# Performance work log

Measured on AMD Instinct MI355X. Metric: run time of the kernel, lower is better.

## Reference

```python
import jax, jax.numpy as jnp
import numpy as np

N, IN_CAPS, IN_LEN = 32, 1152, 32
OUT_CAPS, OUT_LEN = 64, 32
NUM_ITERATIONS = 3


def setup_inputs() -> dict:
    key = jax.random.key(0)
    k1, k2 = jax.random.split(key)
    x = jax.random.normal(k1, (N, IN_CAPS, IN_LEN), dtype=jnp.float32)
    # learnable weight, torch.randn init: (out_capsules, out_length, in_length)
    weight = jax.random.normal(k2, (OUT_CAPS, OUT_LEN, IN_LEN), dtype=jnp.float32)
    return {"x": x, "weight": weight}


def _squash(v):
    # v * ||v|| / (1 + ||v||^2)  ==  (||v||^2/(1+||v||^2)) * v/||v||
    norm_sq = jnp.sum(v * v, axis=-1, keepdims=True)
    norm = jnp.sqrt(norm_sq)
    return v * norm / (1.0 + norm_sq)


def reference(x, weight):
    # priors u_hat: [N, out_caps, in_caps, out_len]
    priors = jnp.einsum('oli,bni->bonl', weight, x)
    logits = jnp.zeros_like(priors)
    output = None
    for r in range(NUM_ITERATIONS):
        # coupling coefficients: softmax over output capsules (axis=1)
        probs = jax.nn.softmax(logits, axis=1)
        # weighted sum over input capsules -> [N, out_caps, 1, out_len]
        output = jnp.sum(probs * priors, axis=-2, keepdims=True)
        if r != NUM_ITERATIONS - 1:
            output = _squash(output)
            # agreement update: [N, out_caps, in_caps, 1]
            logits = logits + jnp.sum(priors * output, axis=-1, keepdims=True)
    output = _squash(output)  # squash=True default
    return jnp.squeeze(output, axis=-2)  # [N, out_caps, out_len]
```

## Files before the change

### kernel.cpp

```cpp
#include <hip/hip_runtime.h>
#include <math.h>


#define N_B      32
#define IN_CAPS  1152
#define IN_LEN   32
#define OUT_CAPS 64
#define OUT_LEN  32

#define NCHUNK 16
#define NPB    (IN_CAPS / NCHUNK)
#define PASS_WAVES 4
#define NPW    (NPB / PASS_WAVES)

#define DPPV(v, ctrl) \
    __int_as_float(__builtin_amdgcn_update_dpp(0, __float_as_int(v), ctrl, 0xF, 0xF, true))

__device__ __forceinline__ float wave_max(float v) {
    v = fmaxf(v, DPPV(v, 0xB1));
    v = fmaxf(v, DPPV(v, 0x4E));
    v = fmaxf(v, DPPV(v, 0x141));
    v = fmaxf(v, DPPV(v, 0x140));
    v = fmaxf(v, __shfl_xor(v, 16, 64));
    v = fmaxf(v, __shfl_xor(v, 32, 64));
    return v;
}
__device__ __forceinline__ float wave_sum(float v) {
    v += DPPV(v, 0xB1);
    v += DPPV(v, 0x4E);
    v += DPPV(v, 0x141);
    v += DPPV(v, 0x140);
    v += __shfl_xor(v, 16, 64);
    v += __shfl_xor(v, 32, 64);
    return v;
}

__global__ __launch_bounds__(256) void k_init(const float* __restrict__ x,
                                              const float* __restrict__ W,
                                              float* __restrict__ T) {
    const int b   = blockIdx.x;
    const int tid = threadIdx.x;
    const float* xb = x + (size_t)b * IN_CAPS * IN_LEN;

    __shared__ float4 red4[32][8];
    {
        const int q = tid & 7;
        const int g = tid >> 3;
        float4 acc = make_float4(0.f, 0.f, 0.f, 0.f);
        for (int n = g; n < IN_CAPS; n += 32) {
            const float4 v = *(const float4*)(xb + n * IN_LEN + q * 4);
            acc.x += v.x; acc.y += v.y; acc.z += v.z; acc.w += v.w;
        }
        red4[g][q] = acc;
    }
    __syncthreads();
    __shared__ float s0[IN_LEN];
    if (tid < 8) {
        float4 v = make_float4(0.f, 0.f, 0.f, 0.f);
        for (int g = 0; g < 32; ++g) {
            const float4 r = red4[g][tid];
            v.x += r.x; v.y += r.y; v.z += r.z; v.w += r.w;
        }
        const float inv = 1.f / 64.f;
        s0[tid * 4 + 0] = v.x * inv;
        s0[tid * 4 + 1] = v.y * inv;
        s0[tid * 4 + 2] = v.z * inv;
        s0[tid * 4 + 3] = v.w * inv;
    }
    __syncthreads();

    __shared__ float u[OUT_CAPS * OUT_LEN];
    for (int e = tid; e < OUT_CAPS * OUT_LEN; e += 256) {
        const float* wrow = W + (size_t)e * IN_LEN;
        float a = 0.f;
#pragma unroll
        for (int i = 0; i < IN_LEN; ++i) a = fmaf(wrow[i], s0[i], a);
        u[e] = a;
    }
    __syncthreads();

    __shared__ float scale[OUT_CAPS];
    if (tid < OUT_CAPS) {
        float ns = 0.f;
#pragma unroll
        for (int l = 0; l < OUT_LEN; ++l) { const float v = u[tid * OUT_LEN + l]; ns = fmaf(v, v, ns); }
        scale[tid] = sqrtf(ns) / (1.f + ns);
    }
    __syncthreads();

    for (int e = tid; e < OUT_CAPS * IN_LEN; e += 256) {
        const int o = e >> 5, i = e & 31;
        float a = 0.f;
#pragma unroll
        for (int l = 0; l < OUT_LEN; ++l)
            a = fmaf(W[((size_t)o * OUT_LEN + l) * IN_LEN + i], u[o * OUT_LEN + l], a);
        T[(size_t)b * OUT_CAPS * IN_LEN + e] = a * scale[o];
    }
}

__global__ __launch_bounds__(256, 2) void k_pass(const float* __restrict__ x,
                                                 const float* __restrict__ T,
                                                 float* __restrict__ part) {
    const int b    = blockIdx.x >> 4;
    const int c    = blockIdx.x & (NCHUNK - 1);
    const int tid  = threadIdx.x;
    const int lane = tid & 63;
    const int wave = __builtin_amdgcn_readfirstlane(tid >> 6);

    float t[IN_LEN];
    {
        const float4* Trow4 = (const float4*)(T + ((size_t)b * OUT_CAPS + lane) * IN_LEN);
#pragma unroll
        for (int q = 0; q < 8; ++q) {
            const float4 v = Trow4[q];
            t[4 * q] = v.x; t[4 * q + 1] = v.y; t[4 * q + 2] = v.z; t[4 * q + 3] = v.w;
        }
    }
    asm volatile("" : "+v"(t[0]), "+v"(t[1]), "+v"(t[2]), "+v"(t[3]),
                      "+v"(t[4]), "+v"(t[5]), "+v"(t[6]), "+v"(t[7]),
                      "+v"(t[8]), "+v"(t[9]), "+v"(t[10]), "+v"(t[11]),
                      "+v"(t[12]), "+v"(t[13]), "+v"(t[14]), "+v"(t[15]));
    asm volatile("" : "+v"(t[16]), "+v"(t[17]), "+v"(t[18]), "+v"(t[19]),
                      "+v"(t[20]), "+v"(t[21]), "+v"(t[22]), "+v"(t[23]),
                      "+v"(t[24]), "+v"(t[25]), "+v"(t[26]), "+v"(t[27]),
                      "+v"(t[28]), "+v"(t[29]), "+v"(t[30]), "+v"(t[31]));

    float s[IN_LEN];
#pragma unroll
    for (int i = 0; i < IN_LEN; ++i) s[i] = 0.f;

    const float* xw = x + ((size_t)b * IN_CAPS + c * NPB + wave * NPW) * IN_LEN;

#define L4(acc, R, k) \
    acc = fmaf((R).x, t[k],     acc); acc = fmaf((R).y, t[k + 1], acc); \
    acc = fmaf((R).z, t[k + 2], acc); acc = fmaf((R).w, t[k + 3], acc);
#define S4(R, k) \
    s[k]     = fmaf(prob, (R).x, s[k]);     s[k + 1] = fmaf(prob, (R).y, s[k + 1]); \
    s[k + 2] = fmaf(prob, (R).z, s[k + 2]); s[k + 3] = fmaf(prob, (R).w, s[k + 3]);

#pragma unroll
    for (int j = 0; j < NPW; ++j) {
        const float4* xr = (const float4*)(xw + j * IN_LEN);
        const float4 r0 = xr[0], r1 = xr[1], r2 = xr[2], r3 = xr[3],
                     r4 = xr[4], r5 = xr[5], r6 = xr[6], r7 = xr[7];

        float l0 = 0.f, l1 = 0.f, l2 = 0.f, l3 = 0.f;
        L4(l0, r0, 0)  L4(l1, r1, 4)  L4(l2, r2, 8)  L4(l3, r3, 12)
        L4(l0, r4, 16) L4(l1, r5, 20) L4(l2, r6, 24) L4(l3, r7, 28)
        const float logit = (l0 + l1) + (l2 + l3);

        const float m = wave_max(logit);
        const float p = __expf(logit - m);
        const float S = wave_sum(p);
        const float prob = p * __builtin_amdgcn_rcpf(S);

        S4(r0, 0)  S4(r1, 4)  S4(r2, 8)  S4(r3, 12)
        S4(r4, 16) S4(r5, 20) S4(r6, 24) S4(r7, 28)
    }
#undef L4
#undef S4

    __shared__ __align__(16) float sp[PASS_WAVES][OUT_CAPS][36];
    {
        float4* dst = (float4*)&sp[wave][lane][0];
#pragma unroll
        for (int q = 0; q < 8; ++q)
            dst[q] = make_float4(s[4 * q], s[4 * q + 1], s[4 * q + 2], s[4 * q + 3]);
    }
    __syncthreads();
    {
        float4* pb4 = (float4*)(part + ((size_t)b * NCHUNK + c) * OUT_CAPS * IN_LEN);
        for (int e = tid; e < OUT_CAPS * IN_LEN / 4; e += 256) {
            const int o = e >> 3, q4 = (e & 7) * 4;
            const float4 a0 = *(const float4*)&sp[0][o][q4];
            const float4 a1 = *(const float4*)&sp[1][o][q4];
            const float4 a2 = *(const float4*)&sp[2][o][q4];
            const float4 a3 = *(const float4*)&sp[3][o][q4];
            pb4[e] = make_float4(a0.x + a1.x + a2.x + a3.x,
                                 a0.y + a1.y + a2.y + a3.y,
                                 a0.z + a1.z + a2.z + a3.z,
                                 a0.w + a1.w + a2.w + a3.w);
        }
    }
}

__global__ __launch_bounds__(256) void k_vt(const float* __restrict__ W,
                                            const float* __restrict__ part,
                                            float* __restrict__ T,
                                            float* __restrict__ out,
                                            int final_iter) {
    const int b   = blockIdx.x;
    const int tid = threadIdx.x;

    __shared__ float s_lds[OUT_CAPS * IN_LEN];
    {
        const float4* pb4 = (const float4*)(part + (size_t)b * NCHUNK * OUT_CAPS * IN_LEN);
        for (int e = tid; e < OUT_CAPS * IN_LEN / 4; e += 256) {
            float4 acc = make_float4(0.f, 0.f, 0.f, 0.f);
#pragma unroll
            for (int c = 0; c < NCHUNK; ++c) {
                const float4 v = pb4[c * (OUT_CAPS * IN_LEN / 4) + e];
                acc.x += v.x; acc.y += v.y; acc.z += v.z; acc.w += v.w;
            }
            ((float4*)s_lds)[e] = acc;
        }
    }
    __syncthreads();

    __shared__ float u[OUT_CAPS * OUT_LEN];
    for (int e = tid; e < OUT_CAPS * OUT_LEN; e += 256) {
        const int o = e >> 5;
        const float* wrow = W + (size_t)e * IN_LEN;
        const float* srow = s_lds + o * IN_LEN;
        float a = 0.f;
#pragma unroll
        for (int i = 0; i < IN_LEN; ++i) a = fmaf(wrow[i], srow[i], a);
        u[e] = a;
    }
    __syncthreads();

    __shared__ float scale[OUT_CAPS];
    if (tid < OUT_CAPS) {
        float ns = 0.f;
#pragma unroll
        for (int l = 0; l < OUT_LEN; ++l) { const float v = u[tid * OUT_LEN + l]; ns = fmaf(v, v, ns); }
        scale[tid] = sqrtf(ns) / (1.f + ns);
    }
    __syncthreads();

    if (final_iter) {
        for (int e = tid; e < OUT_CAPS * OUT_LEN; e += 256)
            out[(size_t)b * OUT_CAPS * OUT_LEN + e] = u[e] * scale[e >> 5];
    } else {
        for (int e = tid; e < OUT_CAPS * IN_LEN; e += 256) {
            const int o = e >> 5, i = e & 31;
            float a = 0.f;
#pragma unroll
            for (int l = 0; l < OUT_LEN; ++l)
                a = fmaf(W[((size_t)o * OUT_LEN + l) * IN_LEN + i], u[o * OUT_LEN + l], a);
            T[(size_t)b * OUT_CAPS * IN_LEN + e] += a * scale[o];
        }
    }
}

extern "C" void kernel_launch(void* const* d_in, const int* in_sizes, int n_in,
                              void* d_out, int out_size, void* d_ws, size_t ws_size,
                              hipStream_t stream) {
    const float* x = (const float*)d_in[0];
    const float* W = (const float*)d_in[1];
    float* out = (float*)d_out;

    float* T    = (float*)d_ws;
    float* part = T + (size_t)N_B * OUT_CAPS * IN_LEN;

    k_init<<<N_B, 256, 0, stream>>>(x, W, T);
    k_pass<<<N_B * NCHUNK, 256, 0, stream>>>(x, T, part);
    k_vt  <<<N_B, 256, 0, stream>>>(W, part, T, out, 0);
    k_pass<<<N_B * NCHUNK, 256, 0, stream>>>(x, T, part);
    k_vt  <<<N_B, 256, 0, stream>>>(W, part, T, out, 1);
}
```

Before: 131.6 us.

## Fuse all routing stages into one cooperative kernel with grid syncs

Replaces five separate kernel launches (init, pass, vt, pass, vt) with a single cooperative kernel of 512 blocks that uses grid.sync between stages. Every block redundantly computes the initial T and the per-batch reduction/update, so T stays in LDS instead of going through global memory. The aim is to remove launch gaps and global round trips, at the cost of 16x redundant init/vt work per batch and two grid-wide barriers. If the cooperative launch fails, the old multi-kernel path is used instead.

```diff
diff --git a/kernel.cpp b/kernel.cpp
--- a/kernel.cpp
+++ b/kernel.cpp
@@ -1,5 +1,8 @@
 #include <hip/hip_runtime.h>
+#include <hip/hip_cooperative_groups.h>
 #include <math.h>
+
+namespace cg = cooperative_groups;
 
 
 #define N_B      32
@@ -12,6 +15,7 @@
 #define NPB    (IN_CAPS / NCHUNK)
 #define PASS_WAVES 4
 #define NPW    (NPB / PASS_WAVES)
+#define TSTR   36
 
 #define DPPV(v, ctrl) \
     __int_as_float(__builtin_amdgcn_update_dpp(0, __float_as_int(v), ctrl, 0xF, 0xF, true))
@@ -35,6 +39,207 @@
     return v;
 }
 
+__global__ __launch_bounds__(256, 2) void k_fused(const float* __restrict__ x,
+                                                  const float* __restrict__ W,
+                                                  float* __restrict__ part,
+                                                  float* __restrict__ out) {
+    const int b    = blockIdx.x >> 4;
+    const int c    = blockIdx.x & (NCHUNK - 1);
+    const int tid  = threadIdx.x;
+    const int lane = tid & 63;
+    const int wave = __builtin_amdgcn_readfirstlane(tid >> 6);
+
+    cg::grid_group grid = cg::this_grid();
+
+    __shared__ __align__(16) float T_lds[OUT_CAPS * TSTR];
+    __shared__ __align__(16) float buf[PASS_WAVES * OUT_CAPS * TSTR];
+
+    {
+        float4* red4 = (float4*)buf;
+        const int q = tid & 7, g = tid >> 3;
+        const float* xb = x + (size_t)b * IN_CAPS * IN_LEN;
+        float4 acc = make_float4(0.f, 0.f, 0.f, 0.f);
+        for (int n = g; n < IN_CAPS; n += 32) {
+            const float4 v = *(const float4*)(xb + n * IN_LEN + q * 4);
+            acc.x += v.x; acc.y += v.y; acc.z += v.z; acc.w += v.w;
+        }
+        red4[g * 8 + q] = acc;
+    }
+    __syncthreads();
+    float* u     = buf + 1024;
+    float* scale = buf + 3072;
+    float* s0    = buf + 3136;
+    if (tid < 8) {
+        const float4* red4 = (const float4*)buf;
+        float4 v = make_float4(0.f, 0.f, 0.f, 0.f);
+        for (int g = 0; g < 32; ++g) {
+            const float4 r = red4[g * 8 + tid];
+            v.x += r.x; v.y += r.y; v.z += r.z; v.w += r.w;
+        }
+        const float inv = 1.f / 64.f;
+        s0[tid * 4 + 0] = v.x * inv;
+        s0[tid * 4 + 1] = v.y * inv;
+        s0[tid * 4 + 2] = v.z * inv;
+        s0[tid * 4 + 3] = v.w * inv;
+    }
+    __syncthreads();
+
+    for (int e = tid; e < OUT_CAPS * OUT_LEN; e += 256) {
+        const float* wrow = W + (size_t)e * IN_LEN;
+        float a = 0.f;
+#pragma unroll
+        for (int i = 0; i < IN_LEN; ++i) a = fmaf(wrow[i], s0[i], a);
+        u[e] = a;
+    }
+    __syncthreads();
+    if (tid < OUT_CAPS) {
+        float ns = 0.f;
+#pragma unroll
+        for (int l = 0; l < OUT_LEN; ++l) { const float v = u[tid * OUT_LEN + l]; ns = fmaf(v, v, ns); }
+        scale[tid] = sqrtf(ns) / (1.f + ns);
+    }
+    __syncthreads();
+    for (int e = tid; e < OUT_CAPS * IN_LEN; e += 256) {
+        const int o = e >> 5, i = e & 31;
+        float a = 0.f;
+#pragma unroll
+        for (int l = 0; l < OUT_LEN; ++l)
+            a = fmaf(W[((size_t)o * OUT_LEN + l) * IN_LEN + i], u[o * OUT_LEN + l], a);
+        T_lds[o * TSTR + i] = a * scale[o];
+    }
+    __syncthreads();
+
+    auto do_pass = [&]() {
+        float t[IN_LEN];
+        {
+#pragma unroll
+            for (int q = 0; q < 8; ++q) {
+                const float4 v = *(const float4*)&T_lds[lane * TSTR + q * 4];
+                t[4 * q] = v.x; t[4 * q + 1] = v.y; t[4 * q + 2] = v.z; t[4 * q + 3] = v.w;
+            }
+        }
+        asm volatile("" : "+v"(t[0]), "+v"(t[1]), "+v"(t[2]), "+v"(t[3]),
+                          "+v"(t[4]), "+v"(t[5]), "+v"(t[6]), "+v"(t[7]),
+                          "+v"(t[8]), "+v"(t[9]), "+v"(t[10]), "+v"(t[11]),
+                          "+v"(t[12]), "+v"(t[13]), "+v"(t[14]), "+v"(t[15]));
+        asm volatile("" : "+v"(t[16]), "+v"(t[17]), "+v"(t[18]), "+v"(t[19]),
+                          "+v"(t[20]), "+v"(t[21]), "+v"(t[22]), "+v"(t[23]),
+                          "+v"(t[24]), "+v"(t[25]), "+v"(t[26]), "+v"(t[27]),
+                          "+v"(t[28]), "+v"(t[29]), "+v"(t[30]), "+v"(t[31]));
+
+        float s[IN_LEN];
+#pragma unroll
+        for (int i = 0; i < IN_LEN; ++i) s[i] = 0.f;
+
+        const float* xw = x + ((size_t)b * IN_CAPS + c * NPB + wave * NPW) * IN_LEN;
+
+#define L4(acc, R, k) \
+    acc = fmaf((R).x, t[k],     acc); acc = fmaf((R).y, t[k + 1], acc); \
+    acc = fmaf((R).z, t[k + 2], acc); acc = fmaf((R).w, t[k + 3], acc);
+#define S4(R, k) \
+    s[k]     = fmaf(prob, (R).x, s[k]);     s[k + 1] = fmaf(prob, (R).y, s[k + 1]); \
+    s[k + 2] = fmaf(prob, (R).z, s[k + 2]); s[k + 3] = fmaf(prob, (R).w, s[k + 3]);
+
+#pragma unroll
+        for (int j = 0; j < NPW; ++j) {
+            const float4* xr = (const float4*)(xw + j * IN_LEN);
+            const float4 r0 = xr[0], r1 = xr[1], r2 = xr[2], r3 = xr[3],
+                         r4 = xr[4], r5 = xr[5], r6 = xr[6], r7 = xr[7];
+
+            float l0 = 0.f, l1 = 0.f, l2 = 0.f, l3 = 0.f;
+            L4(l0, r0, 0)  L4(l1, r1, 4)  L4(l2, r2, 8)  L4(l3, r3, 12)
+            L4(l0, r4, 16) L4(l1, r5, 20) L4(l2, r6, 24) L4(l3, r7, 28)
+            const float logit = (l0 + l1) + (l2 + l3);
+
+            const float m = wave_max(logit);
+            const float p = __expf(logit - m);
+            const float S = wave_sum(p);
+            const float prob = p * __builtin_amdgcn_rcpf(S);
+
+            S4(r0, 0)  S4(r1, 4)  S4(r2, 8)  S4(r3, 12)
+            S4(r4, 16) S4(r5, 20) S4(r6, 24) S4(r7, 28)
+        }
+#undef L4
+#undef S4
+
+        {
+            float4* dst = (float4*)&buf[(wave * OUT_CAPS + lane) * TSTR];
+#pragma unroll
+            for (int q = 0; q < 8; ++q)
+                dst[q] = make_float4(s[4 * q], s[4 * q + 1], s[4 * q + 2], s[4 * q + 3]);
+        }
+        __syncthreads();
+        {
+            float4* pb4 = (float4*)(part + ((size_t)b * NCHUNK + c) * OUT_CAPS * IN_LEN);
+            for (int e = tid; e < OUT_CAPS * IN_LEN / 4; e += 256) {
+                const int o = e >> 3, q4 = (e & 7) * 4;
+                const float4 a0 = *(const float4*)&buf[(0 * OUT_CAPS + o) * TSTR + q4];
+                const float4 a1 = *(const float4*)&buf[(1 * OUT_CAPS + o) * TSTR + q4];
+                const float4 a2 = *(const float4*)&buf[(2 * OUT_CAPS + o) * TSTR + q4];
+                const float4 a3 = *(const float4*)&buf[(3 * OUT_CAPS + o) * TSTR + q4];
+                pb4[e] = make_float4(a0.x + a1.x + a2.x + a3.x,
+                                     a0.y + a1.y + a2.y + a3.y,
+                                     a0.z + a1.z + a2.z + a3.z,
+                                     a0.w + a1.w + a2.w + a3.w);
+            }
+        }
+    };
+
+    float* s_lds = buf;
+    float* uu    = buf + 2048;
+    float* sc    = buf + 4096;
+    auto do_vt_reduce = [&]() {
+        const float4* pb4 = (const float4*)(part + (size_t)b * NCHUNK * OUT_CAPS * IN_LEN);
+        for (int e = tid; e < OUT_CAPS * IN_LEN / 4; e += 256) {
+            float4 acc = make_float4(0.f, 0.f, 0.f, 0.f);
+#pragma unroll
+            for (int cc = 0; cc < NCHUNK; ++cc) {
+                const float4 v = pb4[cc * (OUT_CAPS * IN_LEN / 4) + e];
+                acc.x += v.x; acc.y += v.y; acc.z += v.z; acc.w += v.w;
+            }
+            ((float4*)s_lds)[e] = acc;
+        }
+        __syncthreads();
+        for (int e = tid; e < OUT_CAPS * OUT_LEN; e += 256) {
+            const int o = e >> 5;
+            const float* wrow = W + (size_t)e * IN_LEN;
+            const float* srow = s_lds + o * IN_LEN;
+            float a = 0.f;
+#pragma unroll
+            for (int i = 0; i < IN_LEN; ++i) a = fmaf(wrow[i], srow[i], a);
+            uu[e] = a;
+        }
+        __syncthreads();
+        if (tid < OUT_CAPS) {
+            float ns = 0.f;
+#pragma unroll
+            for (int l = 0; l < OUT_LEN; ++l) { const float v = uu[tid * OUT_LEN + l]; ns = fmaf(v, v, ns); }
+            sc[tid] = sqrtf(ns) / (1.f + ns);
+        }
+        __syncthreads();
+    };
+
+    do_pass();
+    grid.sync();
+    do_vt_reduce();
+    for (int e = tid; e < OUT_CAPS * IN_LEN; e += 256) {
+        const int o = e >> 5, i = e & 31;
+        float a = 0.f;
+#pragma unroll
+        for (int l = 0; l < OUT_LEN; ++l)
+            a = fmaf(W[((size_t)o * OUT_LEN + l) * IN_LEN + i], uu[o * OUT_LEN + l], a);
+        T_lds[o * TSTR + i] += a * sc[o];
+    }
+    __syncthreads();
+
+    do_pass();
+    grid.sync();
+    if (c != 0) return;
+    do_vt_reduce();
+    for (int e = tid; e < OUT_CAPS * OUT_LEN; e += 256)
+        out[(size_t)b * OUT_CAPS * OUT_LEN + e] = uu[e] * sc[e >> 5];
+}
+
 __global__ __launch_bounds__(256) void k_init(const float* __restrict__ x,
                                               const float* __restrict__ W,
                                               float* __restrict__ T) {
@@ -160,7 +365,7 @@
 #undef L4
 #undef S4
 
-    __shared__ __align__(16) float sp[PASS_WAVES][OUT_CAPS][36];
+    __shared__ __align__(16) float sp[PASS_WAVES][OUT_CAPS][TSTR];
     {
         float4* dst = (float4*)&sp[wave][lane][0];
 #pragma unroll
@@ -253,9 +458,15 @@
     float* T    = (float*)d_ws;
     float* part = T + (size_t)N_B * OUT_CAPS * IN_LEN;
 
-    k_init<<<N_B, 256, 0, stream>>>(x, W, T);
-    k_pass<<<N_B * NCHUNK, 256, 0, stream>>>(x, T, part);
-    k_vt  <<<N_B, 256, 0, stream>>>(W, part, T, out, 0);
-    k_pass<<<N_B * NCHUNK, 256, 0, stream>>>(x, T, part);
-    k_vt  <<<N_B, 256, 0, stream>>>(W, part, T, out, 1);
-}
+    void* args[] = { (void*)&x, (void*)&W, (void*)&part, (void*)&out };
+    hipError_t err = hipLaunchCooperativeKernel((const void*)k_fused,
+                                                dim3(N_B * NCHUNK), dim3(256),
+                                                args, 0, stream);
+    if (err != hipSuccess) {
+        k_init<<<N_B, 256, 0, stream>>>(x, W, T);
+        k_pass<<<N_B * NCHUNK, 256, 0, stream>>>(x, T, part);
+        k_vt  <<<N_B, 256, 0, stream>>>(W, part, T, out, 0);
+        k_pass<<<N_B * NCHUNK, 256, 0, stream>>>(x, T, part);
+        k_vt  <<<N_B, 256, 0, stream>>>(W, part, T, out, 1);
+    }
+}
```

Measured after the change: 280.3 us. 113% more time.

## Fuse T computation into pass kernels redundantly per chunk, cut launches to three

Applied to the files above, without the earlier changes.

Fuses the per-batch T computation (init and the mid-iteration vote/squash update) into the chunked pass kernels. Every chunk block recomputes T redundantly and keeps it in LDS, and chunk 0 writes T back for the next stage. The final reduction and squash kernel is spread over 8 blocks per batch with shuffle-based norm reduction. This removes two launches and the low-parallelism 32-block kernels, at the cost of 16x redundant recomputation of the init work (full x reduction per block) and of the W-based matvecs.

```diff
diff --git a/kernel.cpp b/kernel.cpp
--- a/kernel.cpp
+++ b/kernel.cpp
@@ -12,6 +12,7 @@
 #define NPB    (IN_CAPS / NCHUNK)
 #define PASS_WAVES 4
 #define NPW    (NPB / PASS_WAVES)
+#define TSTR   36
 
 #define DPPV(v, ctrl) \
     __int_as_float(__builtin_amdgcn_update_dpp(0, __float_as_int(v), ctrl, 0xF, 0xF, true))
@@ -35,84 +36,15 @@
     return v;
 }
 
-__global__ __launch_bounds__(256) void k_init(const float* __restrict__ x,
-                                              const float* __restrict__ W,
-                                              float* __restrict__ T) {
-    const int b   = blockIdx.x;
-    const int tid = threadIdx.x;
-    const float* xb = x + (size_t)b * IN_CAPS * IN_LEN;
-
-    __shared__ float4 red4[32][8];
-    {
-        const int q = tid & 7;
-        const int g = tid >> 3;
-        float4 acc = make_float4(0.f, 0.f, 0.f, 0.f);
-        for (int n = g; n < IN_CAPS; n += 32) {
-            const float4 v = *(const float4*)(xb + n * IN_LEN + q * 4);
-            acc.x += v.x; acc.y += v.y; acc.z += v.z; acc.w += v.w;
-        }
-        red4[g][q] = acc;
-    }
-    __syncthreads();
-    __shared__ float s0[IN_LEN];
-    if (tid < 8) {
-        float4 v = make_float4(0.f, 0.f, 0.f, 0.f);
-        for (int g = 0; g < 32; ++g) {
-            const float4 r = red4[g][tid];
-            v.x += r.x; v.y += r.y; v.z += r.z; v.w += r.w;
-        }
-        const float inv = 1.f / 64.f;
-        s0[tid * 4 + 0] = v.x * inv;
-        s0[tid * 4 + 1] = v.y * inv;
-        s0[tid * 4 + 2] = v.z * inv;
-        s0[tid * 4 + 3] = v.w * inv;
-    }
-    __syncthreads();
-
-    __shared__ float u[OUT_CAPS * OUT_LEN];
-    for (int e = tid; e < OUT_CAPS * OUT_LEN; e += 256) {
-        const float* wrow = W + (size_t)e * IN_LEN;
-        float a = 0.f;
-#pragma unroll
-        for (int i = 0; i < IN_LEN; ++i) a = fmaf(wrow[i], s0[i], a);
-        u[e] = a;
-    }
-    __syncthreads();
-
-    __shared__ float scale[OUT_CAPS];
-    if (tid < OUT_CAPS) {
-        float ns = 0.f;
-#pragma unroll
-        for (int l = 0; l < OUT_LEN; ++l) { const float v = u[tid * OUT_LEN + l]; ns = fmaf(v, v, ns); }
-        scale[tid] = sqrtf(ns) / (1.f + ns);
-    }
-    __syncthreads();
-
-    for (int e = tid; e < OUT_CAPS * IN_LEN; e += 256) {
-        const int o = e >> 5, i = e & 31;
-        float a = 0.f;
-#pragma unroll
-        for (int l = 0; l < OUT_LEN; ++l)
-            a = fmaf(W[((size_t)o * OUT_LEN + l) * IN_LEN + i], u[o * OUT_LEN + l], a);
-        T[(size_t)b * OUT_CAPS * IN_LEN + e] = a * scale[o];
-    }
-}
-
-__global__ __launch_bounds__(256, 2) void k_pass(const float* __restrict__ x,
-                                                 const float* __restrict__ T,
-                                                 float* __restrict__ part) {
-    const int b    = blockIdx.x >> 4;
-    const int c    = blockIdx.x & (NCHUNK - 1);
-    const int tid  = threadIdx.x;
-    const int lane = tid & 63;
-    const int wave = __builtin_amdgcn_readfirstlane(tid >> 6);
-
+__device__ __forceinline__ void pass_and_flush(const float* __restrict__ x,
+                                               const float* T_lds, float* buf,
+                                               float* __restrict__ part,
+                                               int b, int c, int tid, int lane, int wave) {
     float t[IN_LEN];
     {
-        const float4* Trow4 = (const float4*)(T + ((size_t)b * OUT_CAPS + lane) * IN_LEN);
 #pragma unroll
         for (int q = 0; q < 8; ++q) {
-            const float4 v = Trow4[q];
+            const float4 v = *(const float4*)&T_lds[lane * TSTR + q * 4];
             t[4 * q] = v.x; t[4 * q + 1] = v.y; t[4 * q + 2] = v.z; t[4 * q + 3] = v.w;
         }
     }
@@ -160,9 +92,8 @@
 #undef L4
 #undef S4
 
-    __shared__ __align__(16) float sp[PASS_WAVES][OUT_CAPS][36];
-    {
-        float4* dst = (float4*)&sp[wave][lane][0];
+    {
+        float4* dst = (float4*)&buf[(wave * OUT_CAPS + lane) * TSTR];
 #pragma unroll
         for (int q = 0; q < 8; ++q)
             dst[q] = make_float4(s[4 * q], s[4 * q + 1], s[4 * q + 2], s[4 * q + 3]);
@@ -172,10 +103,10 @@
         float4* pb4 = (float4*)(part + ((size_t)b * NCHUNK + c) * OUT_CAPS * IN_LEN);
         for (int e = tid; e < OUT_CAPS * IN_LEN / 4; e += 256) {
             const int o = e >> 3, q4 = (e & 7) * 4;
-            const float4 a0 = *(const float4*)&sp[0][o][q4];
-            const float4 a1 = *(const float4*)&sp[1][o][q4];
-            const float4 a2 = *(const float4*)&sp[2][o][q4];
-            const float4 a3 = *(const float4*)&sp[3][o][q4];
+            const float4 a0 = *(const float4*)&buf[(0 * OUT_CAPS + o) * TSTR + q4];
+            const float4 a1 = *(const float4*)&buf[(1 * OUT_CAPS + o) * TSTR + q4];
+            const float4 a2 = *(const float4*)&buf[(2 * OUT_CAPS + o) * TSTR + q4];
+            const float4 a3 = *(const float4*)&buf[(3 * OUT_CAPS + o) * TSTR + q4];
             pb4[e] = make_float4(a0.x + a1.x + a2.x + a3.x,
                                  a0.y + a1.y + a2.y + a3.y,
                                  a0.z + a1.z + a2.z + a3.z,
@@ -184,30 +115,112 @@
     }
 }
 
-__global__ __launch_bounds__(256) void k_vt(const float* __restrict__ W,
-                                            const float* __restrict__ part,
-                                            float* __restrict__ T,
-                                            float* __restrict__ out,
-                                            int final_iter) {
-    const int b   = blockIdx.x;
-    const int tid = threadIdx.x;
-
-    __shared__ float s_lds[OUT_CAPS * IN_LEN];
+__global__ __launch_bounds__(256, 2) void kA(const float* __restrict__ x,
+                                             const float* __restrict__ W,
+                                             float* __restrict__ T,
+                                             float* __restrict__ part) {
+    const int b    = blockIdx.x >> 4;
+    const int c    = blockIdx.x & (NCHUNK - 1);
+    const int tid  = threadIdx.x;
+    const int lane = tid & 63;
+    const int wave = __builtin_amdgcn_readfirstlane(tid >> 6);
+
+    __shared__ __align__(16) float T_lds[OUT_CAPS * TSTR];
+    __shared__ __align__(16) float buf[PASS_WAVES * OUT_CAPS * TSTR];
+
+    {
+        float4* red4 = (float4*)buf;
+        const int q = tid & 7, g = tid >> 3;
+        const float* xb = x + (size_t)b * IN_CAPS * IN_LEN;
+        float4 acc = make_float4(0.f, 0.f, 0.f, 0.f);
+        for (int n = g; n < IN_CAPS; n += 32) {
+            const float4 v = *(const float4*)(xb + n * IN_LEN + q * 4);
+            acc.x += v.x; acc.y += v.y; acc.z += v.z; acc.w += v.w;
+        }
+        red4[g * 8 + q] = acc;
+    }
+    __syncthreads();
+    float* u     = buf + 1024;
+    float* scale = buf + 3072;
+    float* s0    = buf + 3136;
+    if (tid < 8) {
+        const float4* red4 = (const float4*)buf;
+        float4 v = make_float4(0.f, 0.f, 0.f, 0.f);
+        for (int g = 0; g < 32; ++g) {
+            const float4 r = red4[g * 8 + tid];
+            v.x += r.x; v.y += r.y; v.z += r.z; v.w += r.w;
+        }
+        const float inv = 1.f / 64.f;
+        s0[tid * 4 + 0] = v.x * inv;
+        s0[tid * 4 + 1] = v.y * inv;
+        s0[tid * 4 + 2] = v.z * inv;
+        s0[tid * 4 + 3] = v.w * inv;
+    }
+    __syncthreads();
+
+    for (int e = tid; e < OUT_CAPS * OUT_LEN; e += 256) {
+        const float* wrow = W + (size_t)e * IN_LEN;
+        float a = 0.f;
+#pragma unroll
+        for (int i = 0; i < IN_LEN; ++i) a = fmaf(wrow[i], s0[i], a);
+        u[e] = a;
+    }
+    __syncthreads();
+    if (tid < OUT_CAPS) {
+        float ns = 0.f;
+#pragma unroll
+        for (int l = 0; l < OUT_LEN; ++l) { const float v = u[tid * OUT_LEN + l]; ns = fmaf(v, v, ns); }
+        scale[tid] = sqrtf(ns) / (1.f + ns);
+    }
+    __syncthreads();
+    for (int e = tid; e < OUT_CAPS * IN_LEN; e += 256) {
+        const int o = e >> 5, i = e & 31;
+        float a = 0.f;
+#pragma unroll
+        for (int l = 0; l < OUT_LEN; ++l)
+            a = fmaf(W[((size_t)o * OUT_LEN + l) * IN_LEN + i], u[o * OUT_LEN + l], a);
+        T_lds[o * TSTR + i] = a * scale[o];
+    }
+    __syncthreads();
+
+    if (c == 0) {
+        for (int e = tid; e < OUT_CAPS * IN_LEN; e += 256)
+            T[(size_t)b * OUT_CAPS * IN_LEN + e] = T_lds[(e >> 5) * TSTR + (e & 31)];
+    }
+
+    pass_and_flush(x, T_lds, buf, part, b, c, tid, lane, wave);
+}
+
+__global__ __launch_bounds__(256, 2) void kB(const float* __restrict__ x,
+                                             const float* __restrict__ W,
+                                             const float* __restrict__ T,
+                                             float* __restrict__ part) {
+    const int b    = blockIdx.x >> 4;
+    const int c    = blockIdx.x & (NCHUNK - 1);
+    const int tid  = threadIdx.x;
+    const int lane = tid & 63;
+    const int wave = __builtin_amdgcn_readfirstlane(tid >> 6);
+
+    __shared__ __align__(16) float T_lds[OUT_CAPS * TSTR];
+    __shared__ __align__(16) float buf[PASS_WAVES * OUT_CAPS * TSTR];
+
+    float* s_lds = buf;
+    float* uu    = buf + 2048;
+    float* sc    = buf + 4096;
+
     {
         const float4* pb4 = (const float4*)(part + (size_t)b * NCHUNK * OUT_CAPS * IN_LEN);
         for (int e = tid; e < OUT_CAPS * IN_LEN / 4; e += 256) {
             float4 acc = make_float4(0.f, 0.f, 0.f, 0.f);
 #pragma unroll
-            for (int c = 0; c < NCHUNK; ++c) {
-                const float4 v = pb4[c * (OUT_CAPS * IN_LEN / 4) + e];
+            for (int cc = 0; cc < NCHUNK; ++cc) {
+                const float4 v = pb4[cc * (OUT_CAPS * IN_LEN / 4) + e];
                 acc.x += v.x; acc.y += v.y; acc.z += v.z; acc.w += v.w;
             }
             ((float4*)s_lds)[e] = acc;
         }
     }
     __syncthreads();
-
-    __shared__ float u[OUT_CAPS * OUT_LEN];
     for (int e = tid; e < OUT_CAPS * OUT_LEN; e += 256) {
         const int o = e >> 5;
         const float* wrow = W + (size_t)e * IN_LEN;
@@ -215,32 +228,63 @@
         float a = 0.f;
 #pragma unroll
         for (int i = 0; i < IN_LEN; ++i) a = fmaf(wrow[i], srow[i], a);
-        u[e] = a;
-    }
-    __syncthreads();
-
-    __shared__ float scale[OUT_CAPS];
+        uu[e] = a;
+    }
+    __syncthreads();
     if (tid < OUT_CAPS) {
         float ns = 0.f;
 #pragma unroll
-        for (int l = 0; l < OUT_LEN; ++l) { const float v = u[tid * OUT_LEN + l]; ns = fmaf(v, v, ns); }
-        scale[tid] = sqrtf(ns) / (1.f + ns);
-    }
-    __syncthreads();
-
-    if (final_iter) {
-        for (int e = tid; e < OUT_CAPS * OUT_LEN; e += 256)
-            out[(size_t)b * OUT_CAPS * OUT_LEN + e] = u[e] * scale[e >> 5];
-    } else {
-        for (int e = tid; e < OUT_CAPS * IN_LEN; e += 256) {
-            const int o = e >> 5, i = e & 31;
-            float a = 0.f;
-#pragma unroll
-            for (int l = 0; l < OUT_LEN; ++l)
-                a = fmaf(W[((size_t)o * OUT_LEN + l) * IN_LEN + i], u[o * OUT_LEN + l], a);
-            T[(size_t)b * OUT_CAPS * IN_LEN + e] += a * scale[o];
-        }
-    }
+        for (int l = 0; l < OUT_LEN; ++l) { const float v = uu[tid * OUT_LEN + l]; ns = fmaf(v, v, ns); }
+        sc[tid] = sqrtf(ns) / (1.f + ns);
+    }
+    __syncthreads();
+
+    for (int e = tid; e < OUT_CAPS * IN_LEN; e += 256) {
+        const int o = e >> 5, i = e & 31;
+        float a = 0.f;
+#pragma unroll
+        for (int l = 0; l < OUT_LEN; ++l)
+            a = fmaf(W[((size_t)o * OUT_LEN + l) * IN_LEN + i], uu[o * OUT_LEN + l], a);
+        T_lds[o * TSTR + i] = T[(size_t)b * OUT_CAPS * IN_LEN + e] + a * sc[o];
+    }
+    __syncthreads();
+
+    pass_and_flush(x, T_lds, buf, part, b, c, tid, lane, wave);
+}
+
+__global__ __launch_bounds__(256) void kC(const float* __restrict__ W,
+                                          const float* __restrict__ part,
+                                          float* __restrict__ out) {
+    const int b   = blockIdx.x >> 3;
+    const int og  = blockIdx.x & 7;
+    const int tid = threadIdx.x;
+    const int ol  = tid >> 5;
+    const int i   = tid & 31;
+    const int o   = og * 8 + ol;
+
+    float a = 0.f;
+    const float* pb = part + (size_t)b * NCHUNK * OUT_CAPS * IN_LEN + o * IN_LEN + i;
+#pragma unroll
+    for (int cc = 0; cc < NCHUNK; ++cc) a += pb[cc * OUT_CAPS * IN_LEN];
+
+    __shared__ float s_lds[8][33];
+    s_lds[ol][i] = a;
+    __syncthreads();
+
+    const float* wrow = W + ((size_t)o * OUT_LEN + i) * IN_LEN;
+    float u = 0.f;
+#pragma unroll
+    for (int k = 0; k < IN_LEN; ++k) u = fmaf(wrow[k], s_lds[ol][k], u);
+
+    float ns = u * u;
+    ns += __shfl_xor(ns, 1, 64);
+    ns += __shfl_xor(ns, 2, 64);
+    ns += __shfl_xor(ns, 4, 64);
+    ns += __shfl_xor(ns, 8, 64);
+    ns += __shfl_xor(ns, 16, 64);
+    const float scale = sqrtf(ns) / (1.f + ns);
+
+    out[((size_t)b * OUT_CAPS + o) * OUT_LEN + i] = u * scale;
 }
 
 extern "C" void kernel_launch(void* const* d_in, const int* in_sizes, int n_in,
@@ -253,9 +297,7 @@
     float* T    = (float*)d_ws;
     float* part = T + (size_t)N_B * OUT_CAPS * IN_LEN;
 
-    k_init<<<N_B, 256, 0, stream>>>(x, W, T);
-    k_pass<<<N_B * NCHUNK, 256, 0, stream>>>(x, T, part);
-    k_vt  <<<N_B, 256, 0, stream>>>(W, part, T, out, 0);
-    k_pass<<<N_B * NCHUNK, 256, 0, stream>>>(x, T, part);
-    k_vt  <<<N_B, 256, 0, stream>>>(W, part, T, out, 1);
-}
+    kA<<<N_B * NCHUNK, 256, 0, stream>>>(x, W, T, part);
+    kB<<<N_B * NCHUNK, 256, 0, stream>>>(x, W, T, part);
+    kC<<<N_B * 8,      256, 0, stream>>>(W, part, out);
+}
```

After: 142.3 us. 8.1% more time.

## Fuse init, routing passes and reductions into one per-batch kernel

Applied to the files above, without the earlier changes.

Replaces the five-kernel sequence with a single kernel of one 512-thread block per batch element. T and the per-wave partial sums stay in LDS instead of going through global workspace. The routing pass now processes four input capsules per step, which gives more independent loads and reductions in flight. This removes launch overhead and global round-trips, but only 32 blocks occupy the GPU compared with 512 before, so parallelism across CUs drops sharply.

```diff
diff --git a/kernel.cpp b/kernel.cpp
--- a/kernel.cpp
+++ b/kernel.cpp
@@ -8,10 +8,11 @@
 #define OUT_CAPS 64
 #define OUT_LEN  32
 
-#define NCHUNK 16
-#define NPB    (IN_CAPS / NCHUNK)
-#define PASS_WAVES 4
-#define NPW    (NPB / PASS_WAVES)
+#define WAVES    8
+#define THREADS  512
+#define NPW      (IN_CAPS / WAVES)
+#define NGRP     (NPW / 4)
+#define TSTR     36
 
 #define DPPV(v, ctrl) \
     __int_as_float(__builtin_amdgcn_update_dpp(0, __float_as_int(v), ctrl, 0xF, 0xF, true))
@@ -35,30 +36,40 @@
     return v;
 }
 
-__global__ __launch_bounds__(256) void k_init(const float* __restrict__ x,
-                                              const float* __restrict__ W,
-                                              float* __restrict__ T) {
-    const int b   = blockIdx.x;
-    const int tid = threadIdx.x;
+__global__ __launch_bounds__(THREADS, 2) void k_all(const float* __restrict__ x,
+                                                    const float* __restrict__ W,
+                                                    float* __restrict__ out) {
+    const int b    = blockIdx.x;
+    const int tid  = threadIdx.x;
+    const int lane = tid & 63;
+    const int wave = __builtin_amdgcn_readfirstlane(tid >> 6);
+
+    __shared__ __align__(16) float T_lds[OUT_CAPS * TSTR];
+    __shared__ __align__(16) float stage[WAVES * OUT_CAPS * TSTR];
+    __shared__ __align__(16) float s_red[OUT_CAPS * TSTR];
+
     const float* xb = x + (size_t)b * IN_CAPS * IN_LEN;
 
-    __shared__ float4 red4[32][8];
+    float4* red4  = (float4*)stage;
+    float*  u     = stage + 2048;
+    float*  scale = stage + 4096;
+    float*  s0    = stage + 4224;
+
     {
-        const int q = tid & 7;
-        const int g = tid >> 3;
+        const int q = tid & 7, g = tid >> 3;
         float4 acc = make_float4(0.f, 0.f, 0.f, 0.f);
-        for (int n = g; n < IN_CAPS; n += 32) {
+        for (int n = g; n < IN_CAPS; n += 64) {
             const float4 v = *(const float4*)(xb + n * IN_LEN + q * 4);
             acc.x += v.x; acc.y += v.y; acc.z += v.z; acc.w += v.w;
         }
-        red4[g][q] = acc;
-    }
-    __syncthreads();
-    __shared__ float s0[IN_LEN];
+        red4[g * 8 + q] = acc;
+    }
+    __syncthreads();
     if (tid < 8) {
         float4 v = make_float4(0.f, 0.f, 0.f, 0.f);
-        for (int g = 0; g < 32; ++g) {
-            const float4 r = red4[g][tid];
+#pragma unroll 16
+        for (int g = 0; g < 64; ++g) {
+            const float4 r = red4[g * 8 + tid];
             v.x += r.x; v.y += r.y; v.z += r.z; v.w += r.w;
         }
         const float inv = 1.f / 64.f;
@@ -69,8 +80,7 @@
     }
     __syncthreads();
 
-    __shared__ float u[OUT_CAPS * OUT_LEN];
-    for (int e = tid; e < OUT_CAPS * OUT_LEN; e += 256) {
+    for (int e = tid; e < OUT_CAPS * OUT_LEN; e += THREADS) {
         const float* wrow = W + (size_t)e * IN_LEN;
         float a = 0.f;
 #pragma unroll
@@ -78,8 +88,6 @@
         u[e] = a;
     }
     __syncthreads();
-
-    __shared__ float scale[OUT_CAPS];
     if (tid < OUT_CAPS) {
         float ns = 0.f;
 #pragma unroll
@@ -87,160 +95,142 @@
         scale[tid] = sqrtf(ns) / (1.f + ns);
     }
     __syncthreads();
-
-    for (int e = tid; e < OUT_CAPS * IN_LEN; e += 256) {
+    for (int e = tid; e < OUT_CAPS * IN_LEN; e += THREADS) {
         const int o = e >> 5, i = e & 31;
         float a = 0.f;
 #pragma unroll
         for (int l = 0; l < OUT_LEN; ++l)
             a = fmaf(W[((size_t)o * OUT_LEN + l) * IN_LEN + i], u[o * OUT_LEN + l], a);
-        T[(size_t)b * OUT_CAPS * IN_LEN + e] = a * scale[o];
-    }
-}
-
-__global__ __launch_bounds__(256, 2) void k_pass(const float* __restrict__ x,
-                                                 const float* __restrict__ T,
-                                                 float* __restrict__ part) {
-    const int b    = blockIdx.x >> 4;
-    const int c    = blockIdx.x & (NCHUNK - 1);
-    const int tid  = threadIdx.x;
-    const int lane = tid & 63;
-    const int wave = __builtin_amdgcn_readfirstlane(tid >> 6);
-
-    float t[IN_LEN];
-    {
-        const float4* Trow4 = (const float4*)(T + ((size_t)b * OUT_CAPS + lane) * IN_LEN);
+        T_lds[o * TSTR + i] = a * scale[o];
+    }
+    __syncthreads();
+
+    auto do_pass = [&]() {
+        float t[IN_LEN];
 #pragma unroll
         for (int q = 0; q < 8; ++q) {
-            const float4 v = Trow4[q];
+            const float4 v = *(const float4*)&T_lds[lane * TSTR + q * 4];
             t[4 * q] = v.x; t[4 * q + 1] = v.y; t[4 * q + 2] = v.z; t[4 * q + 3] = v.w;
         }
-    }
-    asm volatile("" : "+v"(t[0]), "+v"(t[1]), "+v"(t[2]), "+v"(t[3]),
-                      "+v"(t[4]), "+v"(t[5]), "+v"(t[6]), "+v"(t[7]),
-                      "+v"(t[8]), "+v"(t[9]), "+v"(t[10]), "+v"(t[11]),
-                      "+v"(t[12]), "+v"(t[13]), "+v"(t[14]), "+v"(t[15]));
-    asm volatile("" : "+v"(t[16]), "+v"(t[17]), "+v"(t[18]), "+v"(t[19]),
-                      "+v"(t[20]), "+v"(t[21]), "+v"(t[22]), "+v"(t[23]),
-                      "+v"(t[24]), "+v"(t[25]), "+v"(t[26]), "+v"(t[27]),
-                      "+v"(t[28]), "+v"(t[29]), "+v"(t[30]), "+v"(t[31]));
-
-    float s[IN_LEN];
-#pragma unroll
-    for (int i = 0; i < IN_LEN; ++i) s[i] = 0.f;
-
-    const float* xw = x + ((size_t)b * IN_CAPS + c * NPB + wave * NPW) * IN_LEN;
-
-#define L4(acc, R, k) \
-    acc = fmaf((R).x, t[k],     acc); acc = fmaf((R).y, t[k + 1], acc); \
-    acc = fmaf((R).z, t[k + 2], acc); acc = fmaf((R).w, t[k + 3], acc);
-#define S4(R, k) \
-    s[k]     = fmaf(prob, (R).x, s[k]);     s[k + 1] = fmaf(prob, (R).y, s[k + 1]); \
-    s[k + 2] = fmaf(prob, (R).z, s[k + 2]); s[k + 3] = fmaf(prob, (R).w, s[k + 3]);
-
-#pragma unroll
-    for (int j = 0; j < NPW; ++j) {
-        const float4* xr = (const float4*)(xw + j * IN_LEN);
-        const float4 r0 = xr[0], r1 = xr[1], r2 = xr[2], r3 = xr[3],
-                     r4 = xr[4], r5 = xr[5], r6 = xr[6], r7 = xr[7];
-
-        float l0 = 0.f, l1 = 0.f, l2 = 0.f, l3 = 0.f;
-        L4(l0, r0, 0)  L4(l1, r1, 4)  L4(l2, r2, 8)  L4(l3, r3, 12)
-        L4(l0, r4, 16) L4(l1, r5, 20) L4(l2, r6, 24) L4(l3, r7, 28)
-        const float logit = (l0 + l1) + (l2 + l3);
-
-        const float m = wave_max(logit);
-        const float p = __expf(logit - m);
-        const float S = wave_sum(p);
-        const float prob = p * __builtin_amdgcn_rcpf(S);
-
-        S4(r0, 0)  S4(r1, 4)  S4(r2, 8)  S4(r3, 12)
-        S4(r4, 16) S4(r5, 20) S4(r6, 24) S4(r7, 28)
-    }
-#undef L4
-#undef S4
-
-    __shared__ __align__(16) float sp[PASS_WAVES][OUT_CAPS][36];
-    {
-        float4* dst = (float4*)&sp[wave][lane][0];
-#pragma unroll
-        for (int q = 0; q < 8; ++q)
-            dst[q] = make_float4(s[4 * q], s[4 * q + 1], s[4 * q + 2], s[4 * q + 3]);
-    }
-    __syncthreads();
-    {
-        float4* pb4 = (float4*)(part + ((size_t)b * NCHUNK + c) * OUT_CAPS * IN_LEN);
-        for (int e = tid; e < OUT_CAPS * IN_LEN / 4; e += 256) {
-            const int o = e >> 3, q4 = (e & 7) * 4;
-            const float4 a0 = *(const float4*)&sp[0][o][q4];
-            const float4 a1 = *(const float4*)&sp[1][o][q4];
-            const float4 a2 = *(const float4*)&sp[2][o][q4];
-            const float4 a3 = *(const float4*)&sp[3][o][q4];
-            pb4[e] = make_float4(a0.x + a1.x + a2.x + a3.x,
-                                 a0.y + a1.y + a2.y + a3.y,
-                                 a0.z + a1.z + a2.z + a3.z,
-                                 a0.w + a1.w + a2.w + a3.w);
-        }
-    }
-}
-
-__global__ __launch_bounds__(256) void k_vt(const float* __restrict__ W,
-                                            const float* __restrict__ part,
-                                            float* __restrict__ T,
-                                            float* __restrict__ out,
-                                            int final_iter) {
-    const int b   = blockIdx.x;
-    const int tid = threadIdx.x;
-
-    __shared__ float s_lds[OUT_CAPS * IN_LEN];
-    {
-        const float4* pb4 = (const float4*)(part + (size_t)b * NCHUNK * OUT_CAPS * IN_LEN);
-        for (int e = tid; e < OUT_CAPS * IN_LEN / 4; e += 256) {
-            float4 acc = make_float4(0.f, 0.f, 0.f, 0.f);
-#pragma unroll
-            for (int c = 0; c < NCHUNK; ++c) {
-                const float4 v = pb4[c * (OUT_CAPS * IN_LEN / 4) + e];
-                acc.x += v.x; acc.y += v.y; acc.z += v.z; acc.w += v.w;
+        asm volatile("" : "+v"(t[0]), "+v"(t[1]), "+v"(t[2]), "+v"(t[3]),
+                          "+v"(t[4]), "+v"(t[5]), "+v"(t[6]), "+v"(t[7]),
+                          "+v"(t[8]), "+v"(t[9]), "+v"(t[10]), "+v"(t[11]),
+                          "+v"(t[12]), "+v"(t[13]), "+v"(t[14]), "+v"(t[15]));
+        asm volatile("" : "+v"(t[16]), "+v"(t[17]), "+v"(t[18]), "+v"(t[19]),
+                          "+v"(t[20]), "+v"(t[21]), "+v"(t[22]), "+v"(t[23]),
+                          "+v"(t[24]), "+v"(t[25]), "+v"(t[26]), "+v"(t[27]),
+                          "+v"(t[28]), "+v"(t[29]), "+v"(t[30]), "+v"(t[31]));
+
+        float s[IN_LEN];
+#pragma unroll
+        for (int i = 0; i < IN_LEN; ++i) s[i] = 0.f;
+
+        const float* xw = xb + (size_t)wave * NPW * IN_LEN;
+
+        for (int g = 0; g < NGRP; ++g) {
+            const float4* xr = (const float4*)(xw + (size_t)g * 4 * IN_LEN);
+            float4 r[4][8];
+#pragma unroll
+            for (int k = 0; k < 4; ++k)
+#pragma unroll
+                for (int q = 0; q < 8; ++q)
+                    r[k][q] = xr[k * 8 + q];
+
+            float lg[4];
+#pragma unroll
+            for (int k = 0; k < 4; ++k) {
+                float a = 0.f;
+#pragma unroll
+                for (int q = 0; q < 8; ++q) {
+                    a = fmaf(r[k][q].x, t[4 * q + 0], a);
+                    a = fmaf(r[k][q].y, t[4 * q + 1], a);
+                    a = fmaf(r[k][q].z, t[4 * q + 2], a);
+                    a = fmaf(r[k][q].w, t[4 * q + 3], a);
+                }
+                lg[k] = a;
             }
-            ((float4*)s_lds)[e] = acc;
-        }
-    }
-    __syncthreads();
-
-    __shared__ float u[OUT_CAPS * OUT_LEN];
-    for (int e = tid; e < OUT_CAPS * OUT_LEN; e += 256) {
-        const int o = e >> 5;
-        const float* wrow = W + (size_t)e * IN_LEN;
-        const float* srow = s_lds + o * IN_LEN;
-        float a = 0.f;
-#pragma unroll
-        for (int i = 0; i < IN_LEN; ++i) a = fmaf(wrow[i], srow[i], a);
-        u[e] = a;
-    }
-    __syncthreads();
-
-    __shared__ float scale[OUT_CAPS];
-    if (tid < OUT_CAPS) {
-        float ns = 0.f;
-#pragma unroll
-        for (int l = 0; l < OUT_LEN; ++l) { const float v = u[tid * OUT_LEN + l]; ns = fmaf(v, v, ns); }
-        scale[tid] = sqrtf(ns) / (1.f + ns);
-    }
-    __syncthreads();
-
-    if (final_iter) {
-        for (int e = tid; e < OUT_CAPS * OUT_LEN; e += 256)
-            out[(size_t)b * OUT_CAPS * OUT_LEN + e] = u[e] * scale[e >> 5];
-    } else {
-        for (int e = tid; e < OUT_CAPS * IN_LEN; e += 256) {
-            const int o = e >> 5, i = e & 31;
+
+            float m[4], p[4], S[4], prob[4];
+#pragma unroll
+            for (int k = 0; k < 4; ++k) m[k] = wave_max(lg[k]);
+#pragma unroll
+            for (int k = 0; k < 4; ++k) p[k] = __expf(lg[k] - m[k]);
+#pragma unroll
+            for (int k = 0; k < 4; ++k) S[k] = wave_sum(p[k]);
+#pragma unroll
+            for (int k = 0; k < 4; ++k) prob[k] = p[k] * __builtin_amdgcn_rcpf(S[k]);
+
+#pragma unroll
+            for (int q = 0; q < 8; ++q)
+#pragma unroll
+                for (int k = 0; k < 4; ++k) {
+                    s[4 * q + 0] = fmaf(prob[k], r[k][q].x, s[4 * q + 0]);
+                    s[4 * q + 1] = fmaf(prob[k], r[k][q].y, s[4 * q + 1]);
+                    s[4 * q + 2] = fmaf(prob[k], r[k][q].z, s[4 * q + 2]);
+                    s[4 * q + 3] = fmaf(prob[k], r[k][q].w, s[4 * q + 3]);
+                }
+        }
+
+        {
+            float4* dst = (float4*)&stage[(wave * OUT_CAPS + lane) * TSTR];
+#pragma unroll
+            for (int q = 0; q < 8; ++q)
+                dst[q] = make_float4(s[4 * q], s[4 * q + 1], s[4 * q + 2], s[4 * q + 3]);
+        }
+        __syncthreads();
+    };
+
+    auto do_vt = [&](int final_iter) {
+        {
+            const int o = tid >> 3, q4 = (tid & 7) * 4;
+            float4 a = make_float4(0.f, 0.f, 0.f, 0.f);
+#pragma unroll
+            for (int w = 0; w < WAVES; ++w) {
+                const float4 v = *(const float4*)&stage[(w * OUT_CAPS + o) * TSTR + q4];
+                a.x += v.x; a.y += v.y; a.z += v.z; a.w += v.w;
+            }
+            *(float4*)&s_red[o * TSTR + q4] = a;
+        }
+        __syncthreads();
+
+        for (int e = tid; e < OUT_CAPS * OUT_LEN; e += THREADS) {
+            const int o = e >> 5;
+            const float* wrow = W + (size_t)e * IN_LEN;
+            const float* srow = s_red + o * TSTR;
             float a = 0.f;
 #pragma unroll
-            for (int l = 0; l < OUT_LEN; ++l)
-                a = fmaf(W[((size_t)o * OUT_LEN + l) * IN_LEN + i], u[o * OUT_LEN + l], a);
-            T[(size_t)b * OUT_CAPS * IN_LEN + e] += a * scale[o];
-        }
-    }
+            for (int i = 0; i < IN_LEN; ++i) a = fmaf(wrow[i], srow[i], a);
+            u[e] = a;
+        }
+        __syncthreads();
+        if (tid < OUT_CAPS) {
+            float ns = 0.f;
+#pragma unroll
+            for (int l = 0; l < OUT_LEN; ++l) { const float v = u[tid * OUT_LEN + l]; ns = fmaf(v, v, ns); }
+            scale[tid] = sqrtf(ns) / (1.f + ns);
+        }
+        __syncthreads();
+
+        if (final_iter) {
+            for (int e = tid; e < OUT_CAPS * OUT_LEN; e += THREADS)
+                out[(size_t)b * OUT_CAPS * OUT_LEN + e] = u[e] * scale[e >> 5];
+        } else {
+            for (int e = tid; e < OUT_CAPS * IN_LEN; e += THREADS) {
+                const int o = e >> 5, i = e & 31;
+                float a = 0.f;
+#pragma unroll
+                for (int l = 0; l < OUT_LEN; ++l)
+                    a = fmaf(W[((size_t)o * OUT_LEN + l) * IN_LEN + i], u[o * OUT_LEN + l], a);
+                T_lds[o * TSTR + i] += a * scale[o];
+            }
+            __syncthreads();
+        }
+    };
+
+    do_pass();
+    do_vt(0);
+    do_pass();
+    do_vt(1);
 }
 
 extern "C" void kernel_launch(void* const* d_in, const int* in_sizes, int n_in,
@@ -249,13 +239,7 @@
     const float* x = (const float*)d_in[0];
     const float* W = (const float*)d_in[1];
     float* out = (float*)d_out;
-
-    float* T    = (float*)d_ws;
-    float* part = T + (size_t)N_B * OUT_CAPS * IN_LEN;
-
-    k_init<<<N_B, 256, 0, stream>>>(x, W, T);
-    k_pass<<<N_B * NCHUNK, 256, 0, stream>>>(x, T, part);
-    k_vt  <<<N_B, 256, 0, stream>>>(W, part, T, out, 0);
-    k_pass<<<N_B * NCHUNK, 256, 0, stream>>>(x, T, part);
-    k_vt  <<<N_B, 256, 0, stream>>>(W, part, T, out, 1);
-}
+    (void)d_ws; (void)ws_size;
+
+    k_all<<<N_B, THREADS, 0, stream>>>(x, W, out);
+}
```

Result: slower. 196.5 us (+49.3%).
